# Performance work log

Hardware: AMD Instinct MI355X
Metric: run time of the kernel (lower is better)

Reference implementation:

```python
import jax, jax.numpy as jnp
from jax import lax
import numpy as np

H, W = 4096, 4096
KH, KW = 15, 15


def setup_inputs() -> dict:
    key = jax.random.key(0)
    kx, kw = jax.random.split(key)
    X = jax.random.normal(kx, (H, W), dtype=jnp.float32)
    weight = jax.random.uniform(kw, (KH, KW), dtype=jnp.float32)
    bias = jnp.zeros((1,), dtype=jnp.float32)
    return {"X": X, "weight": weight, "bias": bias}


def reference(X, weight, bias):
    # Valid 2D cross-correlation (no kernel flip), matching corr2d.
    # lax.conv_general_dilated performs cross-correlation by default.
    out = lax.conv_general_dilated(
        X[None, None, :, :],            # NCHW: [1, 1, H, W]
        weight[None, None, :, :],       # OIHW: [1, 1, KH, KW]
        window_strides=(1, 1),
        padding="VALID",
    )
    return out[0, 0] + bias[0]          # [H-KH+1, W-KW+1]
```

## Files before the change

### kernel.cpp

```cpp
#include <hip/hip_runtime.h>
#include <hip/hip_bf16.h>

#define H_IN 4096
#define W_IN 4096
#define KH 15
#define KW 15
#define OH (H_IN - KH + 1)
#define OW (W_IN - KW + 1)

#define BM 64
#define BN 128
#define NJ (BN / 16)
#define SROWS (BM + KH - 1)
#define SGROW 18
#define SSTR  192
#define STAGE_N (SROWS * SGROW)
#define NIT 6

typedef __attribute__((ext_vector_type(8))) short short8;
typedef __attribute__((ext_vector_type(4))) float f32x4;

__device__ __forceinline__ ushort f2bf(float f) {
    __hip_bfloat16 h = __float2bfloat16(f);
    return __builtin_bit_cast(ushort, h);
}

__global__ __launch_bounds__(256)
void build_wfrags(const float* __restrict__ Wt, ushort* __restrict__ Bw)
{
    int idx = blockIdx.x * 256 + threadIdx.x;
    if (idx < KH * 64) {
        int kh = idx >> 6, l = idx & 63;
        int j = l & 15, k0 = (l >> 4) * 8;
        union { ushort u[8]; uint4 v; } t;
#pragma unroll
        for (int u = 0; u < 8; ++u) {
            int kw = k0 + u - j;
            t.u[u] = f2bf((kw >= 0 && kw < KW) ? Wt[kh * KW + kw] : 0.0f);
        }
        *reinterpret_cast<uint4*>(&Bw[idx * 8]) = t.v;
    }
}

__global__ __launch_bounds__(256, 4)
void conv2d_mfma_bf16(const float* __restrict__ X,
                      const ushort* __restrict__ Bw,
                      const float* __restrict__ Bias,
                      float* __restrict__ Out)
{
    __shared__ ushort s_x[SROWS * SSTR];

    const int tid = threadIdx.x;
    const int l = tid & 63;
    const int w = tid >> 6;
    const int ox0 = blockIdx.x * BN;
    const int oy0 = blockIdx.y * BM;
    const bool xint = (ox0 + SGROW * 8 <= W_IN);

    float4 v[2 * NIT];
#pragma unroll
    for (int k = 0; k < NIT; ++k) {
        int i = tid + 256 * k;
        if (i < STAGE_N) {
            int r = i / SGROW;
            int g = i % SGROW;
            int gy = min(oy0 + r, H_IN - 1);
            const float* rp = X + (size_t)gy * W_IN;
            int gx = ox0 + g * 8;
            if (xint) {
                v[2 * k + 0] = *reinterpret_cast<const float4*>(rp + gx);
                v[2 * k + 1] = *reinterpret_cast<const float4*>(rp + gx + 4);
            } else {
                v[2 * k + 0].x = rp[min(gx + 0, W_IN - 1)];
                v[2 * k + 0].y = rp[min(gx + 1, W_IN - 1)];
                v[2 * k + 0].z = rp[min(gx + 2, W_IN - 1)];
                v[2 * k + 0].w = rp[min(gx + 3, W_IN - 1)];
                v[2 * k + 1].x = rp[min(gx + 4, W_IN - 1)];
                v[2 * k + 1].y = rp[min(gx + 5, W_IN - 1)];
                v[2 * k + 1].z = rp[min(gx + 6, W_IN - 1)];
                v[2 * k + 1].w = rp[min(gx + 7, W_IN - 1)];
            }
        }
    }
#pragma unroll
    for (int k = 0; k < NIT; ++k) {
        int i = tid + 256 * k;
        if (i < STAGE_N) {
            int r = i / SGROW;
            int g = i % SGROW;
            uint4 pk;
            pk.x = (uint32_t)f2bf(v[2 * k + 0].x) | ((uint32_t)f2bf(v[2 * k + 0].y) << 16);
            pk.y = (uint32_t)f2bf(v[2 * k + 0].z) | ((uint32_t)f2bf(v[2 * k + 0].w) << 16);
            pk.z = (uint32_t)f2bf(v[2 * k + 1].x) | ((uint32_t)f2bf(v[2 * k + 1].y) << 16);
            pk.w = (uint32_t)f2bf(v[2 * k + 1].z) | ((uint32_t)f2bf(v[2 * k + 1].w) << 16);
            *reinterpret_cast<uint4*>(&s_x[r * SSTR + ((g ^ (r & 7)) << 3)]) = pk;
        }
    }
    __syncthreads();

    const ushort* const bbase = Bw + l * 8;
    short8 bfr[KH];
#pragma unroll
    for (int kh = 0; kh < KH; ++kh)
        bfr[kh] = *reinterpret_cast<const short8*>(bbase + kh * 64 * 8);
    __builtin_amdgcn_sched_barrier(0);

    const int r0  = w * 16 + (l & 15);
    const int gc0 = l >> 4;

    f32x4 acc[NJ];
#pragma unroll
    for (int j = 0; j < NJ; ++j) acc[j] = (f32x4){0.f, 0.f, 0.f, 0.f};

#pragma unroll
    for (int kh = 0; kh < KH; ++kh) {
        const int rr = r0 + kh;
        const int rowb = rr * SSTR;
        const int x7 = rr & 7;
#pragma unroll
        for (int j = 0; j < NJ; ++j) {
            int off = rowb + (((gc0 + 2 * j) ^ x7) << 3);
            short8 a = *reinterpret_cast<const short8*>(&s_x[off]);
            acc[j] = __builtin_amdgcn_mfma_f32_16x16x32_bf16(a, bfr[kh], acc[j], 0, 0, 0);
        }
    }

    const float b = Bias[0];
    const int orow0 = oy0 + w * 16 + (l >> 4) * 4;
    const int ocol  = ox0 + (l & 15);
    if (oy0 + BM <= OH && ox0 + BN <= OW) {
        float* op0 = &Out[(size_t)orow0 * OW + ocol];
#pragma unroll
        for (int j = 0; j < NJ; ++j) {
#pragma unroll
            for (int r = 0; r < 4; ++r)
                op0[(size_t)r * OW + j * 16] = acc[j][r] + b;
        }
    } else {
#pragma unroll
        for (int j = 0; j < NJ; ++j) {
            int oc = ocol + j * 16;
            if (oc < OW) {
#pragma unroll
                for (int r = 0; r < 4; ++r) {
                    int orow = orow0 + r;
                    if (orow < OH)
                        Out[(size_t)orow * OW + oc] = acc[j][r] + b;
                }
            }
        }
    }
}

extern "C" void kernel_launch(void* const* d_in, const int* in_sizes, int n_in,
                              void* d_out, int out_size, void* d_ws, size_t ws_size,
                              hipStream_t stream)
{
    const float* X    = (const float*)d_in[0];
    const float* Wt   = (const float*)d_in[1];
    const float* Bias = (const float*)d_in[2];
    float* Out        = (float*)d_out;
    ushort* Bw        = (ushort*)d_ws;

    hipLaunchKernelGGL(build_wfrags, dim3((KH * 64 + 255) / 256), dim3(256), 0, stream,
                       Wt, Bw);

    dim3 grid((OW + BN - 1) / BN,
              (OH + BM - 1) / BM);
    dim3 block(256);
    hipLaunchKernelGGL(conv2d_mfma_bf16, grid, block, 0, stream, X, Bw, Bias, Out);
}
```

Measured before the change: 52.87 us.

## Fuse weight-fragment build into conv kernel and pipeline two row tiles per block

Removes the separate weight-fragment kernel launch; each block now builds the bf16 weight fragments in shared memory itself. Each block processes two vertical output tiles, prefetching the next tile's input into registers while computing the current one. The XOR swizzle is replaced by a padded stride of 152, and B fragments are read from LDS per kh instead of being held in registers. This trades redundant per-block weight building, extra LDS traffic and barriers for one fewer launch and overlap of global loads with MFMA work.

```diff
diff --git a/kernel.cpp b/kernel.cpp
--- a/kernel.cpp
+++ b/kernel.cpp
@@ -13,9 +13,10 @@
 #define NJ (BN / 16)
 #define SROWS (BM + KH - 1)
 #define SGROW 18
-#define SSTR  192
+#define SSTR  152
 #define STAGE_N (SROWS * SGROW)
 #define NIT 6
+#define TPB 2
 
 typedef __attribute__((ext_vector_type(8))) short short8;
 typedef __attribute__((ext_vector_type(4))) float f32x4;
@@ -25,46 +26,17 @@
     return __builtin_bit_cast(ushort, h);
 }
 
-__global__ __launch_bounds__(256)
-void build_wfrags(const float* __restrict__ Wt, ushort* __restrict__ Bw)
+__device__ __forceinline__ void stage_issue(const float* __restrict__ X,
+                                            int iy0, int ox0, bool xint,
+                                            int tid, float4 (&v)[2 * NIT])
 {
-    int idx = blockIdx.x * 256 + threadIdx.x;
-    if (idx < KH * 64) {
-        int kh = idx >> 6, l = idx & 63;
-        int j = l & 15, k0 = (l >> 4) * 8;
-        union { ushort u[8]; uint4 v; } t;
-#pragma unroll
-        for (int u = 0; u < 8; ++u) {
-            int kw = k0 + u - j;
-            t.u[u] = f2bf((kw >= 0 && kw < KW) ? Wt[kh * KW + kw] : 0.0f);
-        }
-        *reinterpret_cast<uint4*>(&Bw[idx * 8]) = t.v;
-    }
-}
-
-__global__ __launch_bounds__(256, 4)
-void conv2d_mfma_bf16(const float* __restrict__ X,
-                      const ushort* __restrict__ Bw,
-                      const float* __restrict__ Bias,
-                      float* __restrict__ Out)
-{
-    __shared__ ushort s_x[SROWS * SSTR];
-
-    const int tid = threadIdx.x;
-    const int l = tid & 63;
-    const int w = tid >> 6;
-    const int ox0 = blockIdx.x * BN;
-    const int oy0 = blockIdx.y * BM;
-    const bool xint = (ox0 + SGROW * 8 <= W_IN);
-
-    float4 v[2 * NIT];
 #pragma unroll
     for (int k = 0; k < NIT; ++k) {
         int i = tid + 256 * k;
         if (i < STAGE_N) {
             int r = i / SGROW;
             int g = i % SGROW;
-            int gy = min(oy0 + r, H_IN - 1);
+            int gy = min(iy0 + r, H_IN - 1);
             const float* rp = X + (size_t)gy * W_IN;
             int gx = ox0 + g * 8;
             if (xint) {
@@ -82,6 +54,11 @@
             }
         }
     }
+}
+
+__device__ __forceinline__ void stage_write(ushort* __restrict__ s_x,
+                                            int tid, const float4 (&v)[2 * NIT])
+{
 #pragma unroll
     for (int k = 0; k < NIT; ++k) {
         int i = tid + 256 * k;
@@ -93,61 +70,102 @@
             pk.y = (uint32_t)f2bf(v[2 * k + 0].z) | ((uint32_t)f2bf(v[2 * k + 0].w) << 16);
             pk.z = (uint32_t)f2bf(v[2 * k + 1].x) | ((uint32_t)f2bf(v[2 * k + 1].y) << 16);
             pk.w = (uint32_t)f2bf(v[2 * k + 1].z) | ((uint32_t)f2bf(v[2 * k + 1].w) << 16);
-            *reinterpret_cast<uint4*>(&s_x[r * SSTR + ((g ^ (r & 7)) << 3)]) = pk;
+            *reinterpret_cast<uint4*>(&s_x[r * SSTR + g * 8]) = pk;
         }
     }
+}
+
+__global__ __launch_bounds__(256, 4)
+void conv2d_mfma_pipe(const float* __restrict__ X,
+                      const float* __restrict__ Wt,
+                      const float* __restrict__ Bias,
+                      float* __restrict__ Out)
+{
+    __shared__ ushort s_w[KH * 64 * 8];
+    __shared__ ushort s_x[SROWS * SSTR];
+
+    const int tid = threadIdx.x;
+    const int l = tid & 63;
+    const int w = tid >> 6;
+    const int ox0 = blockIdx.x * BN;
+    const int ty0 = blockIdx.y * TPB;
+    const bool xint = (ox0 + SGROW * 8 <= W_IN);
+    const float b = Bias[0];
+
+    float4 v[2 * NIT];
+
+    stage_issue(X, ty0 * BM, ox0, xint, tid, v);
+
+    for (int idx = tid; idx < KH * 64; idx += 256) {
+        int kh = idx >> 6, ll = idx & 63;
+        int j = ll & 15, k0 = (ll >> 4) * 8;
+        union { ushort u[8]; uint4 q; } t;
+#pragma unroll
+        for (int u = 0; u < 8; ++u) {
+            int kw = k0 + u - j;
+            t.u[u] = f2bf((kw >= 0 && kw < KW) ? Wt[kh * KW + kw] : 0.0f);
+        }
+        *reinterpret_cast<uint4*>(&s_w[idx * 8]) = t.q;
+    }
+
+    stage_write(s_x, tid, v);
     __syncthreads();
 
-    const ushort* const bbase = Bw + l * 8;
-    short8 bfr[KH];
-#pragma unroll
-    for (int kh = 0; kh < KH; ++kh)
-        bfr[kh] = *reinterpret_cast<const short8*>(bbase + kh * 64 * 8);
-    __builtin_amdgcn_sched_barrier(0);
-
-    const int r0  = w * 16 + (l & 15);
-    const int gc0 = l >> 4;
-
-    f32x4 acc[NJ];
-#pragma unroll
-    for (int j = 0; j < NJ; ++j) acc[j] = (f32x4){0.f, 0.f, 0.f, 0.f};
+    const ushort* const abase = &s_x[(w * 16 + (l & 15)) * SSTR + (l >> 4) * 8];
+    const ushort* const bbase = &s_w[l * 8];
 
 #pragma unroll
-    for (int kh = 0; kh < KH; ++kh) {
-        const int rr = r0 + kh;
-        const int rowb = rr * SSTR;
-        const int x7 = rr & 7;
+    for (int t = 0; t < TPB; ++t) {
+        const int oy0 = (ty0 + t) * BM;
+
+        if (t + 1 < TPB)
+            stage_issue(X, (ty0 + t + 1) * BM, ox0, xint, tid, v);
+        __builtin_amdgcn_sched_barrier(0);
+
+        f32x4 acc[NJ];
 #pragma unroll
-        for (int j = 0; j < NJ; ++j) {
-            int off = rowb + (((gc0 + 2 * j) ^ x7) << 3);
-            short8 a = *reinterpret_cast<const short8*>(&s_x[off]);
-            acc[j] = __builtin_amdgcn_mfma_f32_16x16x32_bf16(a, bfr[kh], acc[j], 0, 0, 0);
+        for (int j = 0; j < NJ; ++j) acc[j] = (f32x4){0.f, 0.f, 0.f, 0.f};
+
+#pragma unroll
+        for (int kh = 0; kh < KH; ++kh) {
+            short8 bf = *reinterpret_cast<const short8*>(bbase + kh * 64 * 8);
+            const ushort* arow = abase + kh * SSTR;
+#pragma unroll
+            for (int j = 0; j < NJ; ++j) {
+                short8 a = *reinterpret_cast<const short8*>(arow + j * 16);
+                acc[j] = __builtin_amdgcn_mfma_f32_16x16x32_bf16(a, bf, acc[j], 0, 0, 0);
+            }
         }
-    }
 
-    const float b = Bias[0];
-    const int orow0 = oy0 + w * 16 + (l >> 4) * 4;
-    const int ocol  = ox0 + (l & 15);
-    if (oy0 + BM <= OH && ox0 + BN <= OW) {
-        float* op0 = &Out[(size_t)orow0 * OW + ocol];
+        const int orow0 = oy0 + w * 16 + (l >> 4) * 4;
+        const int ocol  = ox0 + (l & 15);
+        if (oy0 + BM <= OH && ox0 + BN <= OW) {
+            float* op0 = &Out[(size_t)orow0 * OW + ocol];
 #pragma unroll
-        for (int j = 0; j < NJ; ++j) {
+            for (int j = 0; j < NJ; ++j) {
 #pragma unroll
-            for (int r = 0; r < 4; ++r)
-                op0[(size_t)r * OW + j * 16] = acc[j][r] + b;
-        }
-    } else {
+                for (int r = 0; r < 4; ++r)
+                    op0[(size_t)r * OW + j * 16] = acc[j][r] + b;
+            }
+        } else {
 #pragma unroll
-        for (int j = 0; j < NJ; ++j) {
-            int oc = ocol + j * 16;
-            if (oc < OW) {
+            for (int j = 0; j < NJ; ++j) {
+                int oc = ocol + j * 16;
+                if (oc < OW) {
 #pragma unroll
-                for (int r = 0; r < 4; ++r) {
-                    int orow = orow0 + r;
-                    if (orow < OH)
-                        Out[(size_t)orow * OW + oc] = acc[j][r] + b;
+                    for (int r = 0; r < 4; ++r) {
+                        int orow = orow0 + r;
+                        if (orow < OH)
+                            Out[(size_t)orow * OW + oc] = acc[j][r] + b;
+                    }
                 }
             }
+        }
+
+        if (t + 1 < TPB) {
+            __syncthreads();
+            stage_write(s_x, tid, v);
+            __syncthreads();
         }
     }
 }
@@ -160,13 +178,9 @@
     const float* Wt   = (const float*)d_in[1];
     const float* Bias = (const float*)d_in[2];
     float* Out        = (float*)d_out;
-    ushort* Bw        = (ushort*)d_ws;
-
-    hipLaunchKernelGGL(build_wfrags, dim3((KH * 64 + 255) / 256), dim3(256), 0, stream,
-                       Wt, Bw);
 
     dim3 grid((OW + BN - 1) / BN,
-              (OH + BM - 1) / BM);
+              (OH + BM * TPB - 1) / (BM * TPB));
     dim3 block(256);
-    hipLaunchKernelGGL(conv2d_mfma_bf16, grid, block, 0, stream, X, Bw, Bias, Out);
+    hipLaunchKernelGGL(conv2d_mfma_pipe, grid, block, 0, stream, X, Wt, Bias, Out);
 }
```

Result: faster. 49.46 us (-6.5%).
